# Optimization experiments

Measured on AMD Instinct MI355X. Metric: run time of the kernel, lower is better.

The kernel has to match this reference:

```python
import jax, jax.numpy as jnp
import numpy as np

HEADS = 8
DIM_HEAD = 32
SCALE = DIM_HEAD ** -0.5


def setup_inputs() -> dict:
    key = jax.random.key(0)
    k1, k2, k3 = jax.random.split(key, 3)
    B, L, H, W, C = 2, 5, 100, 176, 256
    inner = HEADS * DIM_HEAD  # 256
    x = jax.random.normal(k1, (B, L, H, W, C), dtype=jnp.float32)
    mask = jnp.ones((B, H, W, 1, L), dtype=jnp.float32)
    W_qkv = jax.random.normal(k2, (C, 3 * inner), dtype=jnp.float32) * (C ** -0.5)
    W_out = jax.random.normal(k3, (inner, C), dtype=jnp.float32) * (inner ** -0.5)
    b_out = jnp.zeros((C,), dtype=jnp.float32)
    return {"x": x, "mask": mask, "W_qkv": W_qkv, "W_out": W_out, "b_out": b_out}


def _cav_attention(x, mask, W_qkv, W_out, b_out):
    B, L, H, W, C = x.shape
    # (B, L, H, W, C) -> (B, H, W, L, C)
    xp = jnp.transpose(x, (0, 2, 3, 1, 4))
    qkv = xp @ W_qkv  # (B,H,W,L,3*inner)
    q, k, v = jnp.split(qkv, 3, axis=-1)

    def to_heads(t):  # (B,H,W,L,m*c) -> (B,m,H,W,L,c)
        t = t.reshape(B, H, W, L, HEADS, DIM_HEAD)
        return jnp.transpose(t, (0, 4, 1, 2, 3, 5))

    q, k, v = to_heads(q), to_heads(k), to_heads(v)
    att = jnp.einsum('bmhwic,bmhwjc->bmhwij', q, k) * SCALE
    # mask: (B,H,W,1,L) -> broadcast over heads as (B,1,H,W,1,L)
    att = jnp.where(mask[:, None] == 0, -jnp.inf, att)
    att = jax.nn.softmax(att, axis=-1)
    out = jnp.einsum('bmhwij,bmhwjc->bmhwic', att, v)
    # (B,m,H,W,L,c) -> (B,H,W,L,m*c)
    out = jnp.transpose(out, (0, 2, 3, 4, 1, 5)).reshape(B, H, W, L, HEADS * DIM_HEAD)
    out = out @ W_out + b_out  # dropout is identity in eval mode
    # (B,H,W,L,C) -> (B,L,H,W,C)
    return jnp.transpose(out, (0, 3, 1, 2, 4))


def reference(x, mask, W_qkv, W_out, b_out):
    return _cav_attention(x, mask, W_qkv, W_out, b_out)
```

## Files before the change

### kernel.cpp

```cpp
#include <hip/hip_runtime.h>
#include <hip/hip_bf16.h>

#define LQ 5
#define HQ 100
#define WQ 176
#define HWQ 17600
#define NT 35200
#define TPB 8
#define ROWS 40
#define NBLK 4400
#define SCALE_QK 0.17677669529663687f

#define AO_OFF 0
#define QBUF_OFF 20480
#define QBUF_STRIDE 7680
#define MASK_OFF 51200
#define GOFS_OFF 51360
#define OBUF_OFF 51520
#define OBUF_WSTRIDE 5120
#define OBUF_HSTRIDE 2560
#define SMEM_BYTES 72512

typedef __attribute__((ext_vector_type(8))) short bf16x8;
typedef __attribute__((ext_vector_type(4))) float f32x4;
typedef __attribute__((ext_vector_type(2))) float f32x2;

__device__ __forceinline__ unsigned short f2bf(float f) {
  __hip_bfloat16 b = __float2bfloat16(f);
  return *(unsigned short*)&b;
}
__device__ __forceinline__ f32x2 bfpair(unsigned w) {
  union { unsigned u; float f; } lo, hi;
  lo.u = w << 16; hi.u = w & 0xffff0000u;
  return (f32x2){lo.f, hi.f};
}
__device__ __forceinline__ unsigned pack2(f32x2 v) {
  return ((unsigned)f2bf(v.y) << 16) | (unsigned)f2bf(v.x);
}
__device__ __forceinline__ int swzA(int row, int b) { return (row * 512 + b) ^ ((row & 7) << 4); }
__device__ __forceinline__ int swzQ(int row, int b) { return (row * 192 + b) ^ ((row & 7) << 4); }
__device__ __forceinline__ int swzO(int row, int b) { return row * 64 + (b ^ ((row & 3) << 4)); }

#if __has_builtin(__builtin_amdgcn_fdot2_f32_bf16)
typedef __attribute__((ext_vector_type(2))) __bf16 bf16x2v;
__device__ __forceinline__ float dot2bf(unsigned a, unsigned b, float c) {
  union { unsigned u; bf16x2v v; } ua, ub;
  ua.u = a; ub.u = b;
  return __builtin_amdgcn_fdot2_f32_bf16(ua.v, ub.v, c, false);
}
#else
__device__ __forceinline__ float dot2bf(unsigned a, unsigned b, float c) {
  f32x2 pa = bfpair(a), pb = bfpair(b);
  return __builtin_fmaf(pa.y, pb.y, __builtin_fmaf(pa.x, pb.x, c));
}
#endif

__global__ void prep_weights(const float* __restrict__ Wqkv,
                             const float* __restrict__ Wout,
                             unsigned short* __restrict__ WqkvT,
                             unsigned short* __restrict__ WoutT) {
  int idx = blockIdx.x * 256 + threadIdx.x;
  if (idx < 256 * 768) {
    int k = idx / 768, n = idx - k * 768;
    WqkvT[n * 256 + k] = f2bf(Wqkv[idx]);
  }
  if (idx < 256 * 256) {
    int k = idx >> 8, n = idx & 255;
    WoutT[n * 256 + k] = f2bf(Wout[idx]);
  }
}

__device__ __forceinline__ void do_head(int head, const char* AO, char* qb, char* ob,
                                        const unsigned short* __restrict__ WqkvT,
                                        const float* maskb,
                                        int lr, int lg, int lane) {
  f32x4 acc[6][3];
  #pragma unroll
  for (int j = 0; j < 6; ++j)
    #pragma unroll
    for (int mt = 0; mt < 3; ++mt)
      acc[j][mt] = (f32x4){0.f, 0.f, 0.f, 0.f};

  const int hb = head * 32;
  const unsigned short* bp[6];
  bp[0] = WqkvT + (hb + lr) * 256 + lg * 8;
  bp[1] = WqkvT + (hb + 16 + lr) * 256 + lg * 8;
  bp[2] = WqkvT + (256 + hb + lr) * 256 + lg * 8;
  bp[3] = WqkvT + (256 + hb + 16 + lr) * 256 + lg * 8;
  bp[4] = WqkvT + (512 + hb + lr) * 256 + lg * 8;
  bp[5] = WqkvT + (512 + hb + 16 + lr) * 256 + lg * 8;

  bf16x8 bb0[6], bb1[6];
  #pragma unroll
  for (int j = 0; j < 6; ++j) {
    bb0[j] = *(const bf16x8*)(bp[j]);
    bb1[j] = *(const bf16x8*)(bp[j] + 32);
  }

  #pragma unroll
  for (int kt = 0; kt < 8; ++kt) {
    bf16x8 a0 = *(const bf16x8*)(AO + swzA(lr,      kt * 64 + lg * 16));
    bf16x8 a1 = *(const bf16x8*)(AO + swzA(16 + lr, kt * 64 + lg * 16));
    bf16x8 a2 = *(const bf16x8*)(AO + swzA(32 + lr, kt * 64 + lg * 16));
    #pragma unroll
    for (int j = 0; j < 6; ++j) {
      bf16x8 bv = (kt & 1) ? bb1[j] : bb0[j];
      acc[j][0] = __builtin_amdgcn_mfma_f32_16x16x32_bf16(a0, bv, acc[j][0], 0, 0, 0);
      acc[j][1] = __builtin_amdgcn_mfma_f32_16x16x32_bf16(a1, bv, acc[j][1], 0, 0, 0);
      acc[j][2] = __builtin_amdgcn_mfma_f32_16x16x32_bf16(a2, bv, acc[j][2], 0, 0, 0);
    }
    if (kt < 6) {
      #pragma unroll
      for (int j = 0; j < 6; ++j) {
        bf16x8 nl = *(const bf16x8*)(bp[j] + (kt + 2) * 32);
        if (kt & 1) bb1[j] = nl; else bb0[j] = nl;
      }
    }
  }

  #pragma unroll
  for (int j = 0; j < 6; ++j)
    #pragma unroll
    for (int mt = 0; mt < 3; ++mt)
      #pragma unroll
      for (int rg = 0; rg < 4; ++rg) {
        int row = mt * 16 + lg * 4 + rg;
        if (row < ROWS)
          *(unsigned short*)(qb + swzQ(row, (j * 16 + lr) * 2)) = f2bf(acc[j][mt][rg]);
      }

  if (lane < ROWS) {
    const int r = lane;
    const int t5 = (r / 5) * 5;
    uint4 q0 = *(const uint4*)(qb + swzQ(r, 0));
    uint4 q1 = *(const uint4*)(qb + swzQ(r, 16));
    uint4 q2 = *(const uint4*)(qb + swzQ(r, 32));
    uint4 q3 = *(const uint4*)(qb + swzQ(r, 48));

    float p[5];
    #pragma unroll
    for (int j = 0; j < 5; ++j) {
      const int rk = t5 + j;
      uint4 k0 = *(const uint4*)(qb + swzQ(rk, 64));
      uint4 k1 = *(const uint4*)(qb + swzQ(rk, 80));
      uint4 k2 = *(const uint4*)(qb + swzQ(rk, 96));
      uint4 k3 = *(const uint4*)(qb + swzQ(rk, 112));
      float d = 0.f;
      d = dot2bf(q0.x, k0.x, d); d = dot2bf(q0.y, k0.y, d);
      d = dot2bf(q0.z, k0.z, d); d = dot2bf(q0.w, k0.w, d);
      d = dot2bf(q1.x, k1.x, d); d = dot2bf(q1.y, k1.y, d);
      d = dot2bf(q1.z, k1.z, d); d = dot2bf(q1.w, k1.w, d);
      d = dot2bf(q2.x, k2.x, d); d = dot2bf(q2.y, k2.y, d);
      d = dot2bf(q2.z, k2.z, d); d = dot2bf(q2.w, k2.w, d);
      d = dot2bf(q3.x, k3.x, d); d = dot2bf(q3.y, k3.y, d);
      d = dot2bf(q3.z, k3.z, d); d = dot2bf(q3.w, k3.w, d);
      p[j] = d * SCALE_QK + maskb[rk];
    }
    float mx = fmaxf(fmaxf(fmaxf(p[0], p[1]), fmaxf(p[2], p[3])), p[4]);
    float sum = 0.f;
    #pragma unroll
    for (int j = 0; j < 5; ++j) { p[j] = __expf(p[j] - mx); sum += p[j]; }
    const float inv = 1.0f / sum;
    #pragma unroll
    for (int j = 0; j < 5; ++j) p[j] *= inv;

    f32x2 o2[16];
    #pragma unroll
    for (int c = 0; c < 16; ++c) o2[c] = (f32x2){0.f, 0.f};
    #pragma unroll
    for (int j = 0; j < 5; ++j) {
      const int rv = t5 + j;
      uint4 v0 = *(const uint4*)(qb + swzQ(rv, 128));
      uint4 v1 = *(const uint4*)(qb + swzQ(rv, 144));
      uint4 v2 = *(const uint4*)(qb + swzQ(rv, 160));
      uint4 v3 = *(const uint4*)(qb + swzQ(rv, 176));
      f32x2 pj2 = (f32x2){p[j], p[j]};
      o2[0]  += pj2 * bfpair(v0.x); o2[1]  += pj2 * bfpair(v0.y);
      o2[2]  += pj2 * bfpair(v0.z); o2[3]  += pj2 * bfpair(v0.w);
      o2[4]  += pj2 * bfpair(v1.x); o2[5]  += pj2 * bfpair(v1.y);
      o2[6]  += pj2 * bfpair(v1.z); o2[7]  += pj2 * bfpair(v1.w);
      o2[8]  += pj2 * bfpair(v2.x); o2[9]  += pj2 * bfpair(v2.y);
      o2[10] += pj2 * bfpair(v2.z); o2[11] += pj2 * bfpair(v2.w);
      o2[12] += pj2 * bfpair(v3.x); o2[13] += pj2 * bfpair(v3.y);
      o2[14] += pj2 * bfpair(v3.z); o2[15] += pj2 * bfpair(v3.w);
    }
    unsigned oPk[16];
    #pragma unroll
    for (int c = 0; c < 16; ++c) oPk[c] = pack2(o2[c]);
    const int sx = (r & 3) << 4;
    *(uint4*)(ob + r * 64 + (0 ^ sx))  = make_uint4(oPk[0],  oPk[1],  oPk[2],  oPk[3]);
    *(uint4*)(ob + r * 64 + (16 ^ sx)) = make_uint4(oPk[4],  oPk[5],  oPk[6],  oPk[7]);
    *(uint4*)(ob + r * 64 + (32 ^ sx)) = make_uint4(oPk[8],  oPk[9],  oPk[10], oPk[11]);
    *(uint4*)(ob + r * 64 + (48 ^ sx)) = make_uint4(oPk[12], oPk[13], oPk[14], oPk[15]);
  }
}

__global__ __launch_bounds__(256, 2)
void cav_attn_fused(const float* __restrict__ x,
                    const float* __restrict__ mask,
                    const unsigned short* __restrict__ WqkvT,
                    const unsigned short* __restrict__ WoutT,
                    const float* __restrict__ b_out,
                    float* __restrict__ out) {
  extern __shared__ char smem[];
  char*  AO    = smem + AO_OFF;
  float* maskb = (float*)(smem + MASK_OFF);
  int*   gofs  = (int*)(smem + GOFS_OFF);

  const int tid  = threadIdx.x;
  const int wave = tid >> 6;
  const int lane = tid & 63;
  const int lr   = lane & 15;
  const int lg   = lane >> 4;
  const int tile0 = blockIdx.x * TPB;

  if (lane < ROWS) {
    int tt = lane / LQ;
    int l  = lane - tt * LQ;
    int gt = tile0 + tt;
    int b  = (gt >= HWQ) ? 1 : 0;
    int rem = gt - b * HWQ;
    gofs[lane] = (((b * LQ + l) * HQ) * WQ + rem) << 8;
    float mv = mask[gt * LQ + l];
    maskb[lane] = (mv == 0.0f) ? -1e30f : 0.0f;
  }

  #pragma unroll
  for (int i = 0; i < 10; ++i) {
    int r = i * 4 + wave;
    f32x4 v = *(const f32x4*)(x + gofs[r] + lane * 4);
    ushort4 pk;
    pk.x = f2bf(v[0]); pk.y = f2bf(v[1]); pk.z = f2bf(v[2]); pk.w = f2bf(v[3]);
    *(ushort4*)(AO + swzA(r, lane * 8)) = pk;
  }
  __syncthreads();

  char* qb = smem + QBUF_OFF + wave * QBUF_STRIDE;
  char* ob = smem + OBUF_OFF + wave * OBUF_WSTRIDE;
  do_head(wave * 2,     AO, qb, ob,                WqkvT, maskb, lr, lg, lane);
  do_head(wave * 2 + 1, AO, qb, ob + OBUF_HSTRIDE, WqkvT, maskb, lr, lg, lane);
  __syncthreads();

  f32x4 acc2[4][3];
  #pragma unroll
  for (int j = 0; j < 4; ++j)
    #pragma unroll
    for (int mt = 0; mt < 3; ++mt)
      acc2[j][mt] = (f32x4){0.f, 0.f, 0.f, 0.f};

  const unsigned short* bp2[4];
  #pragma unroll
  for (int j = 0; j < 4; ++j)
    bp2[j] = WoutT + (wave * 64 + j * 16 + lr) * 256 + lg * 8;

  bf16x8 cc0[4], cc1[4];
  #pragma unroll
  for (int j = 0; j < 4; ++j) {
    cc0[j] = *(const bf16x8*)(bp2[j]);
    cc1[j] = *(const bf16x8*)(bp2[j] + 32);
  }

  #pragma unroll
  for (int kt = 0; kt < 8; ++kt) {
    const char* OB = smem + OBUF_OFF + (kt >> 1) * OBUF_WSTRIDE + (kt & 1) * OBUF_HSTRIDE;
    bf16x8 a0 = *(const bf16x8*)(OB + swzO(lr,      lg * 16));
    bf16x8 a1 = *(const bf16x8*)(OB + swzO(16 + lr, lg * 16));
    bf16x8 a2 = *(const bf16x8*)(OB + swzO(32 + lr, lg * 16));
    #pragma unroll
    for (int j = 0; j < 4; ++j) {
      bf16x8 bv = (kt & 1) ? cc1[j] : cc0[j];
      acc2[j][0] = __builtin_amdgcn_mfma_f32_16x16x32_bf16(a0, bv, acc2[j][0], 0, 0, 0);
      acc2[j][1] = __builtin_amdgcn_mfma_f32_16x16x32_bf16(a1, bv, acc2[j][1], 0, 0, 0);
      acc2[j][2] = __builtin_amdgcn_mfma_f32_16x16x32_bf16(a2, bv, acc2[j][2], 0, 0, 0);
    }
    if (kt < 6) {
      #pragma unroll
      for (int j = 0; j < 4; ++j) {
        bf16x8 nl = *(const bf16x8*)(bp2[j] + (kt + 2) * 32);
        if (kt & 1) cc1[j] = nl; else cc0[j] = nl;
      }
    }
  }

  #pragma unroll
  for (int j = 0; j < 4; ++j) {
    const int col = wave * 64 + j * 16 + lr;
    const float bo = b_out[col];
    #pragma unroll
    for (int mt = 0; mt < 3; ++mt)
      #pragma unroll
      for (int rg = 0; rg < 4; ++rg) {
        int row = mt * 16 + lg * 4 + rg;
        if (row < ROWS)
          out[gofs[row] + col] = acc2[j][mt][rg] + bo;
      }
  }
}

extern "C" void kernel_launch(void* const* d_in, const int* in_sizes, int n_in,
                              void* d_out, int out_size, void* d_ws, size_t ws_size,
                              hipStream_t stream) {
  (void)in_sizes; (void)n_in; (void)out_size; (void)ws_size;
  const float* x    = (const float*)d_in[0];
  const float* mask = (const float*)d_in[1];
  const float* Wqkv = (const float*)d_in[2];
  const float* Wout = (const float*)d_in[3];
  const float* bout = (const float*)d_in[4];
  float* out = (float*)d_out;

  unsigned short* WqkvT = (unsigned short*)d_ws;
  unsigned short* WoutT = WqkvT + 768 * 256;

  (void)hipFuncSetAttribute((const void*)cav_attn_fused,
                            hipFuncAttributeMaxDynamicSharedMemorySize, SMEM_BYTES);

  prep_weights<<<768, 256, 0, stream>>>(Wqkv, Wout, WqkvT, WoutT);
  cav_attn_fused<<<NBLK, 256, SMEM_BYTES, stream>>>(x, mask, WqkvT, WoutT, bout, out);
}
```

Baseline: 348.2 us.

## Compute attention scores and PV via block-diagonal MFMA instead of scalar dot products

Replaces the per-lane scalar QK dot products and PV accumulation with MFMA matmuls over the full 40x40 tile. Masking outside each 5x5 diagonal block is applied before a shuffle-based softmax. Q/K results are stored transposed in a packed layout so they can be reused as MFMA fragments. The attention output goes back into the input buffer in shared memory for the output projection, and the final stores become f32x4 vectors with vectorized bias loads. The aim is to move attention work onto the matrix cores, make global stores wider and cut shared memory. The cost is wasted MFMA work on the zero off-diagonal blocks and an extra barrier.

```diff
diff --git a/kernel.cpp b/kernel.cpp
--- a/kernel.cpp
+++ b/kernel.cpp
@@ -2,8 +2,6 @@
 #include <hip/hip_bf16.h>
 
 #define LQ 5
-#define HQ 100
-#define WQ 176
 #define HWQ 17600
 #define NT 35200
 #define TPB 8
@@ -12,48 +10,25 @@
 #define SCALE_QK 0.17677669529663687f
 
 #define AO_OFF 0
-#define QBUF_OFF 20480
-#define QBUF_STRIDE 7680
-#define MASK_OFF 51200
-#define GOFS_OFF 51360
-#define OBUF_OFF 51520
-#define OBUF_WSTRIDE 5120
-#define OBUF_HSTRIDE 2560
-#define SMEM_BYTES 72512
+#define WAVE_OFF 20480
+#define WAVE_STRIDE 10368
+#define VT_OFF 5760
+#define GOFS_OFF 61952
+#define MASK_OFF 62144
+#define SMEM_BYTES 62336
 
 typedef __attribute__((ext_vector_type(8))) short bf16x8;
 typedef __attribute__((ext_vector_type(4))) float f32x4;
-typedef __attribute__((ext_vector_type(2))) float f32x2;
 
 __device__ __forceinline__ unsigned short f2bf(float f) {
   __hip_bfloat16 b = __float2bfloat16(f);
   return *(unsigned short*)&b;
 }
-__device__ __forceinline__ f32x2 bfpair(unsigned w) {
-  union { unsigned u; float f; } lo, hi;
-  lo.u = w << 16; hi.u = w & 0xffff0000u;
-  return (f32x2){lo.f, hi.f};
-}
-__device__ __forceinline__ unsigned pack2(f32x2 v) {
-  return ((unsigned)f2bf(v.y) << 16) | (unsigned)f2bf(v.x);
+__device__ __forceinline__ unsigned pack2(float a, float b) {
+  return ((unsigned)f2bf(b) << 16) | (unsigned)f2bf(a);
 }
 __device__ __forceinline__ int swzA(int row, int b) { return (row * 512 + b) ^ ((row & 7) << 4); }
-__device__ __forceinline__ int swzQ(int row, int b) { return (row * 192 + b) ^ ((row & 7) << 4); }
-__device__ __forceinline__ int swzO(int row, int b) { return row * 64 + (b ^ ((row & 3) << 4)); }
-
-#if __has_builtin(__builtin_amdgcn_fdot2_f32_bf16)
-typedef __attribute__((ext_vector_type(2))) __bf16 bf16x2v;
-__device__ __forceinline__ float dot2bf(unsigned a, unsigned b, float c) {
-  union { unsigned u; bf16x2v v; } ua, ub;
-  ua.u = a; ub.u = b;
-  return __builtin_amdgcn_fdot2_f32_bf16(ua.v, ub.v, c, false);
-}
-#else
-__device__ __forceinline__ float dot2bf(unsigned a, unsigned b, float c) {
-  f32x2 pa = bfpair(a), pb = bfpair(b);
-  return __builtin_fmaf(pa.y, pb.y, __builtin_fmaf(pa.x, pb.x, c));
-}
-#endif
+__device__ __forceinline__ int swzR(int row, int off) { return row * 144 + (off ^ ((row & 3) << 4)); }
 
 __global__ void prep_weights(const float* __restrict__ Wqkv,
                              const float* __restrict__ Wout,
@@ -70,17 +45,11 @@
   }
 }
 
-__device__ __forceinline__ void do_head(int head, const char* AO, char* qb, char* ob,
+__device__ __forceinline__ void do_head(int head, const char* AO, char* qkp, char* vt,
                                         const unsigned short* __restrict__ WqkvT,
-                                        const float* maskb,
-                                        int lr, int lg, int lane) {
-  f32x4 acc[6][3];
-  #pragma unroll
-  for (int j = 0; j < 6; ++j)
-    #pragma unroll
-    for (int mt = 0; mt < 3; ++mt)
-      acc[j][mt] = (f32x4){0.f, 0.f, 0.f, 0.f};
-
+                                        const f32x4* mrg ,
+                                        int lr, int lg, int lane,
+                                        f32x4* oacc ) {
   const int hb = head * 32;
   const unsigned short* bp[6];
   bp[0] = WqkvT + (hb + lr) * 256 + lg * 8;
@@ -90,6 +59,16 @@
   bp[4] = WqkvT + (512 + hb + lr) * 256 + lg * 8;
   bp[5] = WqkvT + (512 + hb + 16 + lr) * 256 + lg * 8;
 
+  f32x4 aqk[4][3], av[2][3];
+  #pragma unroll
+  for (int j = 0; j < 4; ++j)
+    #pragma unroll
+    for (int g = 0; g < 3; ++g) aqk[j][g] = (f32x4){0.f, 0.f, 0.f, 0.f};
+  #pragma unroll
+  for (int j = 0; j < 2; ++j)
+    #pragma unroll
+    for (int g = 0; g < 3; ++g) av[j][g] = (f32x4){0.f, 0.f, 0.f, 0.f};
+
   bf16x8 bb0[6], bb1[6];
   #pragma unroll
   for (int j = 0; j < 6; ++j) {
@@ -99,15 +78,22 @@
 
   #pragma unroll
   for (int kt = 0; kt < 8; ++kt) {
-    bf16x8 a0 = *(const bf16x8*)(AO + swzA(lr,      kt * 64 + lg * 16));
-    bf16x8 a1 = *(const bf16x8*)(AO + swzA(16 + lr, kt * 64 + lg * 16));
-    bf16x8 a2 = *(const bf16x8*)(AO + swzA(32 + lr, kt * 64 + lg * 16));
-    #pragma unroll
-    for (int j = 0; j < 6; ++j) {
-      bf16x8 bv = (kt & 1) ? bb1[j] : bb0[j];
-      acc[j][0] = __builtin_amdgcn_mfma_f32_16x16x32_bf16(a0, bv, acc[j][0], 0, 0, 0);
-      acc[j][1] = __builtin_amdgcn_mfma_f32_16x16x32_bf16(a1, bv, acc[j][1], 0, 0, 0);
-      acc[j][2] = __builtin_amdgcn_mfma_f32_16x16x32_bf16(a2, bv, acc[j][2], 0, 0, 0);
+    bf16x8 xf0 = *(const bf16x8*)(AO + swzA(lr,      kt * 64 + lg * 16));
+    bf16x8 xf1 = *(const bf16x8*)(AO + swzA(16 + lr, kt * 64 + lg * 16));
+    bf16x8 xf2 = *(const bf16x8*)(AO + swzA(32 + lr, kt * 64 + lg * 16));
+    #pragma unroll
+    for (int j = 0; j < 4; ++j) {
+      bf16x8 w = (kt & 1) ? bb1[j] : bb0[j];
+      aqk[j][0] = __builtin_amdgcn_mfma_f32_16x16x32_bf16(w, xf0, aqk[j][0], 0, 0, 0);
+      aqk[j][1] = __builtin_amdgcn_mfma_f32_16x16x32_bf16(w, xf1, aqk[j][1], 0, 0, 0);
+      aqk[j][2] = __builtin_amdgcn_mfma_f32_16x16x32_bf16(w, xf2, aqk[j][2], 0, 0, 0);
+    }
+    #pragma unroll
+    for (int j = 0; j < 2; ++j) {
+      bf16x8 w = (kt & 1) ? bb1[4 + j] : bb0[4 + j];
+      av[j][0] = __builtin_amdgcn_mfma_f32_16x16x32_bf16(xf0, w, av[j][0], 0, 0, 0);
+      av[j][1] = __builtin_amdgcn_mfma_f32_16x16x32_bf16(xf1, w, av[j][1], 0, 0, 0);
+      av[j][2] = __builtin_amdgcn_mfma_f32_16x16x32_bf16(xf2, w, av[j][2], 0, 0, 0);
     }
     if (kt < 6) {
       #pragma unroll
@@ -119,79 +105,96 @@
   }
 
   #pragma unroll
-  for (int j = 0; j < 6; ++j)
-    #pragma unroll
-    for (int mt = 0; mt < 3; ++mt)
-      #pragma unroll
-      for (int rg = 0; rg < 4; ++rg) {
-        int row = mt * 16 + lg * 4 + rg;
-        if (row < ROWS)
-          *(unsigned short*)(qb + swzQ(row, (j * 16 + lr) * 2)) = f2bf(acc[j][mt][rg]);
-      }
+  for (int j = 0; j < 4; ++j)
+    #pragma unroll
+    for (int g = 0; g < 3; ++g) {
+      int sp = g * 16 + lr;
+      if (sp < ROWS) {
+        uint2 w;
+        w.x = pack2(aqk[j][g][0], aqk[j][g][1]);
+        w.y = pack2(aqk[j][g][2], aqk[j][g][3]);
+        int off = (j & 1) * 32 + lg * 8 + ((j >= 2) ? 64 : 0);
+        *(uint2*)(qkp + swzR(sp, off)) = w;
+      }
+    }
+  #pragma unroll
+  for (int j = 0; j < 2; ++j)
+    #pragma unroll
+    for (int g = 0; g < 3; ++g) {
+      if (g < 2 || lg < 2) {
+        uint2 w;
+        w.x = pack2(av[j][g][0], av[j][g][1]);
+        w.y = pack2(av[j][g][2], av[j][g][3]);
+        *(uint2*)(vt + swzR(j * 16 + lr, g * 32 + lg * 8)) = w;
+      }
+    }
+
+  bf16x8 kf0 = *(const bf16x8*)(qkp + swzR(lr,      64 + lg * 16));
+  bf16x8 kf1 = *(const bf16x8*)(qkp + swzR(16 + lr, 64 + lg * 16));
+  bf16x8 kf2 = *(const bf16x8*)(qkp + swzR(32 + lr, 64 + lg * 16));
+  f32x4 sa[3][3];
+  #pragma unroll
+  for (int gq = 0; gq < 3; ++gq) {
+    bf16x8 qf = *(const bf16x8*)(qkp + swzR(gq * 16 + lr, lg * 16));
+    sa[gq][0] = __builtin_amdgcn_mfma_f32_16x16x32_bf16(kf0, qf, (f32x4){0.f,0.f,0.f,0.f}, 0, 0, 0);
+    sa[gq][1] = __builtin_amdgcn_mfma_f32_16x16x32_bf16(kf1, qf, (f32x4){0.f,0.f,0.f,0.f}, 0, 0, 0);
+    sa[gq][2] = __builtin_amdgcn_mfma_f32_16x16x32_bf16(kf2, qf, (f32x4){0.f,0.f,0.f,0.f}, 0, 0, 0);
+  }
 
   if (lane < ROWS) {
-    const int r = lane;
-    const int t5 = (r / 5) * 5;
-    uint4 q0 = *(const uint4*)(qb + swzQ(r, 0));
-    uint4 q1 = *(const uint4*)(qb + swzQ(r, 16));
-    uint4 q2 = *(const uint4*)(qb + swzQ(r, 32));
-    uint4 q3 = *(const uint4*)(qb + swzQ(r, 48));
-
-    float p[5];
-    #pragma unroll
-    for (int j = 0; j < 5; ++j) {
-      const int rk = t5 + j;
-      uint4 k0 = *(const uint4*)(qb + swzQ(rk, 64));
-      uint4 k1 = *(const uint4*)(qb + swzQ(rk, 80));
-      uint4 k2 = *(const uint4*)(qb + swzQ(rk, 96));
-      uint4 k3 = *(const uint4*)(qb + swzQ(rk, 112));
-      float d = 0.f;
-      d = dot2bf(q0.x, k0.x, d); d = dot2bf(q0.y, k0.y, d);
-      d = dot2bf(q0.z, k0.z, d); d = dot2bf(q0.w, k0.w, d);
-      d = dot2bf(q1.x, k1.x, d); d = dot2bf(q1.y, k1.y, d);
-      d = dot2bf(q1.z, k1.z, d); d = dot2bf(q1.w, k1.w, d);
-      d = dot2bf(q2.x, k2.x, d); d = dot2bf(q2.y, k2.y, d);
-      d = dot2bf(q2.z, k2.z, d); d = dot2bf(q2.w, k2.w, d);
-      d = dot2bf(q3.x, k3.x, d); d = dot2bf(q3.y, k3.y, d);
-      d = dot2bf(q3.z, k3.z, d); d = dot2bf(q3.w, k3.w, d);
-      p[j] = d * SCALE_QK + maskb[rk];
-    }
-    float mx = fmaxf(fmaxf(fmaxf(p[0], p[1]), fmaxf(p[2], p[3])), p[4]);
-    float sum = 0.f;
-    #pragma unroll
-    for (int j = 0; j < 5; ++j) { p[j] = __expf(p[j] - mx); sum += p[j]; }
-    const float inv = 1.0f / sum;
-    #pragma unroll
-    for (int j = 0; j < 5; ++j) p[j] *= inv;
-
-    f32x2 o2[16];
-    #pragma unroll
-    for (int c = 0; c < 16; ++c) o2[c] = (f32x2){0.f, 0.f};
-    #pragma unroll
-    for (int j = 0; j < 5; ++j) {
-      const int rv = t5 + j;
-      uint4 v0 = *(const uint4*)(qb + swzQ(rv, 128));
-      uint4 v1 = *(const uint4*)(qb + swzQ(rv, 144));
-      uint4 v2 = *(const uint4*)(qb + swzQ(rv, 160));
-      uint4 v3 = *(const uint4*)(qb + swzQ(rv, 176));
-      f32x2 pj2 = (f32x2){p[j], p[j]};
-      o2[0]  += pj2 * bfpair(v0.x); o2[1]  += pj2 * bfpair(v0.y);
-      o2[2]  += pj2 * bfpair(v0.z); o2[3]  += pj2 * bfpair(v0.w);
-      o2[4]  += pj2 * bfpair(v1.x); o2[5]  += pj2 * bfpair(v1.y);
-      o2[6]  += pj2 * bfpair(v1.z); o2[7]  += pj2 * bfpair(v1.w);
-      o2[8]  += pj2 * bfpair(v2.x); o2[9]  += pj2 * bfpair(v2.y);
-      o2[10] += pj2 * bfpair(v2.z); o2[11] += pj2 * bfpair(v2.w);
-      o2[12] += pj2 * bfpair(v3.x); o2[13] += pj2 * bfpair(v3.y);
-      o2[14] += pj2 * bfpair(v3.z); o2[15] += pj2 * bfpair(v3.w);
-    }
-    unsigned oPk[16];
-    #pragma unroll
-    for (int c = 0; c < 16; ++c) oPk[c] = pack2(o2[c]);
-    const int sx = (r & 3) << 4;
-    *(uint4*)(ob + r * 64 + (0 ^ sx))  = make_uint4(oPk[0],  oPk[1],  oPk[2],  oPk[3]);
-    *(uint4*)(ob + r * 64 + (16 ^ sx)) = make_uint4(oPk[4],  oPk[5],  oPk[6],  oPk[7]);
-    *(uint4*)(ob + r * 64 + (32 ^ sx)) = make_uint4(oPk[8],  oPk[9],  oPk[10], oPk[11]);
-    *(uint4*)(ob + r * 64 + (48 ^ sx)) = make_uint4(oPk[12], oPk[13], oPk[14], oPk[15]);
+    *(uint4*)(qkp + swzR(lane, 96))  = make_uint4(0, 0, 0, 0);
+    *(uint4*)(qkp + swzR(lane, 112)) = make_uint4(0, 0, 0, 0);
+  }
+
+  #pragma unroll
+  for (int gq = 0; gq < 3; ++gq) {
+    int q = gq * 16 + lr;
+    int t5 = (q / 5) * 5;
+    float v[3][4];
+    #pragma unroll
+    for (int gk = 0; gk < 3; ++gk)
+      #pragma unroll
+      for (int r = 0; r < 4; ++r) {
+        int k = gk * 16 + lg * 4 + r;
+        float raw = sa[gq][gk][r] * SCALE_QK + mrg[gk][r];
+        v[gk][r] = ((unsigned)(k - t5) < 5u) ? raw : -1e30f;
+      }
+    float m = v[0][0];
+    #pragma unroll
+    for (int gk = 0; gk < 3; ++gk)
+      #pragma unroll
+      for (int r = 0; r < 4; ++r) m = fmaxf(m, v[gk][r]);
+    m = fmaxf(m, __shfl_xor(m, 16));
+    m = fmaxf(m, __shfl_xor(m, 32));
+    float e[3][4], s = 0.f;
+    #pragma unroll
+    for (int gk = 0; gk < 3; ++gk)
+      #pragma unroll
+      for (int r = 0; r < 4; ++r) { e[gk][r] = __expf(v[gk][r] - m); s += e[gk][r]; }
+    s += __shfl_xor(s, 16);
+    s += __shfl_xor(s, 32);
+    float inv = 1.0f / s;
+    if (q < ROWS) {
+      #pragma unroll
+      for (int gk = 0; gk < 3; ++gk) {
+        uint2 w;
+        w.x = pack2(e[gk][0] * inv, e[gk][1] * inv);
+        w.y = pack2(e[gk][2] * inv, e[gk][3] * inv);
+        *(uint2*)(qkp + swzR(q, gk * 32 + lg * 8)) = w;
+      }
+    }
+  }
+
+  #pragma unroll
+  for (int kt = 0; kt < 2; ++kt) {
+    bf16x8 vf0 = *(const bf16x8*)(vt + swzR(lr,      kt * 64 + lg * 16));
+    bf16x8 vf1 = *(const bf16x8*)(vt + swzR(16 + lr, kt * 64 + lg * 16));
+    #pragma unroll
+    for (int gq = 0; gq < 3; ++gq) {
+      bf16x8 pf = *(const bf16x8*)(qkp + swzR(gq * 16 + lr, kt * 64 + lg * 16));
+      oacc[gq * 2 + 0] = __builtin_amdgcn_mfma_f32_16x16x32_bf16(pf, vf0, oacc[gq * 2 + 0], 0, 0, 0);
+      oacc[gq * 2 + 1] = __builtin_amdgcn_mfma_f32_16x16x32_bf16(pf, vf1, oacc[gq * 2 + 1], 0, 0, 0);
+    }
   }
 }
 
@@ -204,8 +207,8 @@
                     float* __restrict__ out) {
   extern __shared__ char smem[];
   char*  AO    = smem + AO_OFF;
+  int*   gofs  = (int*)(smem + GOFS_OFF);
   float* maskb = (float*)(smem + MASK_OFF);
-  int*   gofs  = (int*)(smem + GOFS_OFF);
 
   const int tid  = threadIdx.x;
   const int wave = tid >> 6;
@@ -214,16 +217,35 @@
   const int lg   = lane >> 4;
   const int tile0 = blockIdx.x * TPB;
 
-  if (lane < ROWS) {
-    int tt = lane / LQ;
-    int l  = lane - tt * LQ;
-    int gt = tile0 + tt;
-    int b  = (gt >= HWQ) ? 1 : 0;
-    int rem = gt - b * HWQ;
-    gofs[lane] = (((b * LQ + l) * HQ) * WQ + rem) << 8;
-    float mv = mask[gt * LQ + l];
-    maskb[lane] = (mv == 0.0f) ? -1e30f : 0.0f;
-  }
+  if (lane < 48) {
+    if (lane < ROWS) {
+      int tt = lane / LQ;
+      int l  = lane - tt * LQ;
+      int gt = tile0 + tt;
+      int b  = (gt >= HWQ) ? 1 : 0;
+      int rem = gt - b * HWQ;
+      gofs[lane]  = (((b * LQ + l) * 100) * 176 + rem) << 8;
+      float mv = mask[tile0 * LQ + lane];
+      maskb[lane] = (mv == 0.0f) ? -1e30f : 0.0f;
+    } else {
+      gofs[lane] = 0;
+      maskb[lane] = 0.0f;
+    }
+  }
+
+  char* qkp = smem + WAVE_OFF + wave * WAVE_STRIDE;
+  char* vt  = qkp + VT_OFF;
+
+  if (lane < 32) {
+    *(uint4*)(vt + swzR(lane, 80))  = make_uint4(0, 0, 0, 0);
+    *(uint4*)(vt + swzR(lane, 96))  = make_uint4(0, 0, 0, 0);
+    *(uint4*)(vt + swzR(lane, 112)) = make_uint4(0, 0, 0, 0);
+  }
+
+  f32x4 mrg[3];
+  #pragma unroll
+  for (int gk = 0; gk < 3; ++gk)
+    mrg[gk] = *(const f32x4*)(maskb + gk * 16 + lg * 4);
 
   #pragma unroll
   for (int i = 0; i < 10; ++i) {
@@ -235,18 +257,35 @@
   }
   __syncthreads();
 
-  char* qb = smem + QBUF_OFF + wave * QBUF_STRIDE;
-  char* ob = smem + OBUF_OFF + wave * OBUF_WSTRIDE;
-  do_head(wave * 2,     AO, qb, ob,                WqkvT, maskb, lr, lg, lane);
-  do_head(wave * 2 + 1, AO, qb, ob + OBUF_HSTRIDE, WqkvT, maskb, lr, lg, lane);
+  f32x4 oacc0[6], oacc1[6];
+  #pragma unroll
+  for (int i = 0; i < 6; ++i) { oacc0[i] = (f32x4){0.f,0.f,0.f,0.f}; oacc1[i] = (f32x4){0.f,0.f,0.f,0.f}; }
+
+  do_head(wave * 2,     AO, qkp, vt, WqkvT, mrg, lr, lg, lane, oacc0);
+  do_head(wave * 2 + 1, AO, qkp, vt, WqkvT, mrg, lr, lg, lane, oacc1);
+
   __syncthreads();
 
+  #pragma unroll
+  for (int gq = 0; gq < 3; ++gq)
+    #pragma unroll
+    for (int nf = 0; nf < 2; ++nf)
+      #pragma unroll
+      for (int rg = 0; rg < 4; ++rg) {
+        int sp = gq * 16 + lg * 4 + rg;
+        if (sp < ROWS) {
+          int fb0 = (wave * 64 + nf * 16 + lr) * 2;
+          *(unsigned short*)(AO + swzA(sp, fb0))      = f2bf(oacc0[gq * 2 + nf][rg]);
+          *(unsigned short*)(AO + swzA(sp, fb0 + 64)) = f2bf(oacc1[gq * 2 + nf][rg]);
+        }
+      }
+  __syncthreads();
+
   f32x4 acc2[4][3];
   #pragma unroll
   for (int j = 0; j < 4; ++j)
     #pragma unroll
-    for (int mt = 0; mt < 3; ++mt)
-      acc2[j][mt] = (f32x4){0.f, 0.f, 0.f, 0.f};
+    for (int g = 0; g < 3; ++g) acc2[j][g] = (f32x4){0.f, 0.f, 0.f, 0.f};
 
   const unsigned short* bp2[4];
   #pragma unroll
@@ -262,16 +301,15 @@
 
   #pragma unroll
   for (int kt = 0; kt < 8; ++kt) {
-    const char* OB = smem + OBUF_OFF + (kt >> 1) * OBUF_WSTRIDE + (kt & 1) * OBUF_HSTRIDE;
-    bf16x8 a0 = *(const bf16x8*)(OB + swzO(lr,      lg * 16));
-    bf16x8 a1 = *(const bf16x8*)(OB + swzO(16 + lr, lg * 16));
-    bf16x8 a2 = *(const bf16x8*)(OB + swzO(32 + lr, lg * 16));
+    bf16x8 of0 = *(const bf16x8*)(AO + swzA(lr,      kt * 64 + lg * 16));
+    bf16x8 of1 = *(const bf16x8*)(AO + swzA(16 + lr, kt * 64 + lg * 16));
+    bf16x8 of2 = *(const bf16x8*)(AO + swzA(32 + lr, kt * 64 + lg * 16));
     #pragma unroll
     for (int j = 0; j < 4; ++j) {
-      bf16x8 bv = (kt & 1) ? cc1[j] : cc0[j];
-      acc2[j][0] = __builtin_amdgcn_mfma_f32_16x16x32_bf16(a0, bv, acc2[j][0], 0, 0, 0);
-      acc2[j][1] = __builtin_amdgcn_mfma_f32_16x16x32_bf16(a1, bv, acc2[j][1], 0, 0, 0);
-      acc2[j][2] = __builtin_amdgcn_mfma_f32_16x16x32_bf16(a2, bv, acc2[j][2], 0, 0, 0);
+      bf16x8 w = (kt & 1) ? cc1[j] : cc0[j];
+      acc2[j][0] = __builtin_amdgcn_mfma_f32_16x16x32_bf16(w, of0, acc2[j][0], 0, 0, 0);
+      acc2[j][1] = __builtin_amdgcn_mfma_f32_16x16x32_bf16(w, of1, acc2[j][1], 0, 0, 0);
+      acc2[j][2] = __builtin_amdgcn_mfma_f32_16x16x32_bf16(w, of2, acc2[j][2], 0, 0, 0);
     }
     if (kt < 6) {
       #pragma unroll
@@ -282,18 +320,22 @@
     }
   }
 
-  #pragma unroll
-  for (int j = 0; j < 4; ++j) {
-    const int col = wave * 64 + j * 16 + lr;
-    const float bo = b_out[col];
-    #pragma unroll
-    for (int mt = 0; mt < 3; ++mt)
-      #pragma unroll
-      for (int rg = 0; rg < 4; ++rg) {
-        int row = mt * 16 + lg * 4 + rg;
-        if (row < ROWS)
-          out[gofs[row] + col] = acc2[j][mt][rg] + bo;
-      }
+  f32x4 bias[4];
+  #pragma unroll
+  for (int j = 0; j < 4; ++j)
+    bias[j] = *(const f32x4*)(b_out + wave * 64 + j * 16 + lg * 4);
+
+  #pragma unroll
+  for (int g = 0; g < 3; ++g) {
+    int sp = g * 16 + lr;
+    if (sp < ROWS) {
+      int go = gofs[sp];
+      #pragma unroll
+      for (int j = 0; j < 4; ++j) {
+        f32x4 v = acc2[j][g] + bias[j];
+        *(f32x4*)(out + go + wave * 64 + j * 16 + lg * 4) = v;
+      }
+    }
   }
 }
 
@@ -311,9 +353,6 @@
   unsigned short* WqkvT = (unsigned short*)d_ws;
   unsigned short* WoutT = WqkvT + 768 * 256;
 
-  (void)hipFuncSetAttribute((const void*)cav_attn_fused,
-                            hipFuncAttributeMaxDynamicSharedMemorySize, SMEM_BYTES);
-
   prep_weights<<<768, 256, 0, stream>>>(Wqkv, Wout, WqkvT, WoutT);
   cav_attn_fused<<<NBLK, 256, SMEM_BYTES, stream>>>(x, mask, WqkvT, WoutT, bout, out);
 }
```

Result: slower. 386.7 us (+11.1%).
